# Performance work log

Measured on AMD Instinct MI355X. Metric: run time of the kernel, lower is better.

The kernel has to match this reference:

```python
import jax, jax.numpy as jnp
import numpy as np

H_HT, W_HT = 26, 122      # downsampled pred grid fed to the Hough transform
NUM_ANGLE = 60            # 180 deg / 3 deg
NUM_RHO = 125             # 2*ceil(diag/2)+1, diag = sqrt(26^2+122^2)


def _make_vote_index():
    # Reproduce the structure of vote_index_26_122_3_1.mat: for each pixel
    # (h, w) and angle a, exactly one rho bin receives a vote of 1.0.
    theta = np.deg2rad(np.arange(NUM_ANGLE) * 3.0)
    ys = np.arange(H_HT) - H_HT / 2.0 + 0.5
    xs = np.arange(W_HT) - W_HT / 2.0 + 0.5
    # rho[h, w, a] = x*cos(theta_a) + y*sin(theta_a)
    rho = xs[None, :, None] * np.cos(theta)[None, None, :] \
        + ys[:, None, None] * np.sin(theta)[None, None, :]
    ri = np.clip(np.round(rho).astype(np.int64) + NUM_RHO // 2, 0, NUM_RHO - 1)
    vote = np.zeros((H_HT, W_HT, NUM_ANGLE, NUM_RHO), dtype=np.float32)
    hh, ww, aa = np.meshgrid(np.arange(H_HT), np.arange(W_HT),
                             np.arange(NUM_ANGLE), indexing='ij')
    vote[hh, ww, aa, ri] = 1.0
    return jnp.asarray(vote)


def setup_inputs() -> dict:
    key = jax.random.key(0)
    k1, k2, k3 = jax.random.split(key, 3)
    B, C = 32, 4
    ht = jax.random.uniform(k1, (B, C, NUM_ANGLE, NUM_RHO), dtype=jnp.float32)
    pred = jax.random.uniform(k2, (B, C, 288, 800), dtype=jnp.float32)
    pred_exist = jax.random.uniform(k3, (B, C), dtype=jnp.float32)
    vote_index = _make_vote_index()
    return {"ht": ht, "pred": pred, "pred_exist": pred_exist,
            "vote_index": vote_index}


def _nearest_resize(x, out_h, out_w):
    # torch F.interpolate(mode='nearest'): src = floor(dst * in/out)
    in_h, in_w = x.shape[2], x.shape[3]
    hi = jnp.floor(jnp.arange(out_h) * (in_h / out_h)).astype(jnp.int32)
    wi = jnp.floor(jnp.arange(out_w) * (in_w / out_w)).astype(jnp.int32)
    return x[:, :, hi][:, :, :, wi]


def reference(ht, pred, pred_exist, vote_index):
    B, C = ht.shape[0], ht.shape[1]
    # --- no_grad block in the original ---
    exist = (pred_exist > 0.9).astype(ht.dtype)          # [B, 4]
    exist = jnp.broadcast_to(exist[:, None, :], (B, C, 4))  # [B, C, 4]
    pred_s = _nearest_resize(pred, H_HT, W_HT)           # [B, C, 26, 122]
    # Hough-transform vote accumulation: gather pixel values into (angle, rho)
    # bins via the one-hot vote_index table.
    pred_ht = jnp.einsum('bchw,hwar->bcar', pred_s, vote_index)  # [B,C,A,R]
    idx = jnp.argmax(pred_ht.reshape(B, C, -1), axis=2)  # [B, 4]
    idx = jnp.broadcast_to(idx[:, None, :], (B, C, 4))   # [B, C, 4]
    # --- differentiable part ---
    # F.normalize(ht, dim=2, p=1): L1-normalize along the angle dim.
    l1 = jnp.sum(jnp.abs(ht), axis=2, keepdims=True)
    ht_n = ht / jnp.maximum(l1, 1e-12)
    flat = ht_n.reshape(B, C, -1)                        # [B, C, A*R]
    gathered = jnp.take_along_axis(flat, idx, axis=2)    # [B, C, 4]
    ht_max_log = -jnp.log(gathered + 1e-12)
    loss = ht_max_log * exist
    return loss.mean(axis=2).mean(axis=1)                # [B]
```

## Files before the change

kernel.cpp:

```cpp
#include <hip/hip_runtime.h>
#include <hip/hip_bf16.h>
#include <stdint.h>
#include <math.h>

#define H_HT 26
#define W_HT 122
#define NPIX (H_HT * W_HT)
#define NA 60
#define NR 125
#define NB 32
#define NC 4
#define NBC (NB * NC)
#define PH 288
#define PW 800
#define NSPLIT 16
#define PIX_PT 13

#define TR_BLKS (H_HT * 8)
#define ZERO_BLKS 4

#define WS_OFF   190336
#define WS_LIST  220608
#define WS_PREDT 601280
#define WS_PVP   2225344

__global__ __launch_bounds__(256) void setup(const float* __restrict__ pred,
                                             int* __restrict__ off,
                                             uint16_t* __restrict__ list,
                                             float* __restrict__ pred_T,
                                             unsigned long long* __restrict__ pvp) {
    const int tid = threadIdx.x;
    if (blockIdx.x < NA) {
        const int a = blockIdx.x;
        __shared__ int s_cnt[NR];
        __shared__ int sc[2][NR];
        __shared__ int s_pre[NR + 1];
        __shared__ int s_cur[NR];

        double t  = __dmul_rn((double)(a * 3), 0.017453292519943295);
        double cs = cos(t);
        double sn = sin(t);

        int rloc[PIX_PT];
#pragma unroll
        for (int k = 0; k < PIX_PT; ++k) {
            int p = tid + k * 256;
            rloc[k] = 0;
            if (p < NPIX) {
                int h = p / W_HT;
                int w = p - h * W_HT;
                double xs = (double)w - 60.5;
                double ys = (double)h - 12.5;
                double rho = __dadd_rn(__dmul_rn(xs, cs), __dmul_rn(ys, sn));
                int r = (int)rint(rho) + NR / 2;
                r = r < 0 ? 0 : (r > NR - 1 ? NR - 1 : r);
                rloc[k] = r;
            }
        }
        for (int i = tid; i < NR; i += 256) s_cnt[i] = 0;
        __syncthreads();
#pragma unroll
        for (int k = 0; k < PIX_PT; ++k) {
            int p = tid + k * 256;
            if (p < NPIX) atomicAdd(&s_cnt[rloc[k]], 1);
        }
        __syncthreads();
        if (tid < NR) sc[0][tid] = s_cnt[tid];
        __syncthreads();
        int pin = 0;
        for (int d = 1; d < NR; d <<= 1) {
            if (tid < NR) {
                int v = sc[pin][tid];
                if (tid >= d) v += sc[pin][tid - d];
                sc[pin ^ 1][tid] = v;
            }
            __syncthreads();
            pin ^= 1;
        }
        if (tid == 0) s_pre[0] = 0;
        if (tid < NR) s_pre[tid + 1] = sc[pin][tid];
        __syncthreads();
        for (int r = tid; r < NR + 1; r += 256) off[a * (NR + 1) + r] = s_pre[r];
        for (int r = tid; r < NR; r += 256) s_cur[r] = s_pre[r];
        __syncthreads();
#pragma unroll
        for (int k = 0; k < PIX_PT; ++k) {
            int p = tid + k * 256;
            if (p < NPIX) {
                int slot = atomicAdd(&s_cur[rloc[k]], 1);
                list[a * NPIX + slot] = (uint16_t)p;
            }
        }
    } else if (blockIdx.x < NA + TR_BLKS) {
        const int bidx = blockIdx.x - NA;
        const int h    = bidx >> 3;
        const int g    = bidx & 7;
        const int bc0  = g * 16;
        __shared__ float s_row[16][802];
        const float C1 = (float)(288.0 / 26.0);
        const float C2 = (float)(800.0 / 122.0);
        const int hi = (int)floorf((float)h * C1);
        for (int i = tid; i < 16 * 200; i += 256) {
            int j  = i / 200;
            int c4 = i - j * 200;
            const float4* rp = reinterpret_cast<const float4*>(
                pred + ((size_t)(bc0 + j) * PH + hi) * PW);
            float4 v = rp[c4];
            s_row[j][c4 * 4 + 0] = v.x;
            s_row[j][c4 * 4 + 1] = v.y;
            s_row[j][c4 * 4 + 2] = v.z;
            s_row[j][c4 * 4 + 3] = v.w;
        }
        __syncthreads();
        for (int idx = tid; idx < W_HT * 16; idx += 256) {
            int w = idx >> 4;
            int j = idx & 15;
            int wi = (int)floorf((float)w * C2);
            pred_T[(size_t)(h * W_HT + w) * NBC + bc0 + j] = s_row[j][wi];
        }
    } else {
        int i0 = (blockIdx.x - NA - TR_BLKS) * 256 + tid;
        for (int i = i0; i < NA * NBC; i += ZERO_BLKS * 256) pvp[i] = 0ull;
    }
}

__global__ __launch_bounds__(256) void hough_T4(const float* __restrict__ pred_T,
                                                const int* __restrict__ off,
                                                const uint16_t* __restrict__ list,
                                                unsigned long long* __restrict__ pvp) {
    __shared__ uint16_t s_list[NPIX];
    __shared__ int      s_off[NR + 1];
    __shared__ float    s_v0[4][64], s_v1[4][64];
    __shared__ int      s_i0[4][64], s_i1[4][64];

    const int blk  = blockIdx.x;
    const int a    = blk / NSPLIT;
    const int q    = blk - a * NSPLIT;
    const int tid  = threadIdx.x;
    const int w    = tid >> 6;
    const int lane = tid & 63;

    {
        const uint32_t* src = reinterpret_cast<const uint32_t*>(list + a * NPIX);
        uint32_t* dst = reinterpret_cast<uint32_t*>(s_list);
        for (int i = tid; i < NPIX / 2; i += 256) dst[i] = src[i];
        for (int r = tid; r < NR + 1; r += 256) s_off[r] = off[a * (NR + 1) + r];
    }
    __syncthreads();

    const float2* pT2 = reinterpret_cast<const float2*>(pred_T);
    float bv0 = -1.0f, bv1 = -1.0f; int bi0 = 0x7fffffff, bi1 = 0x7fffffff;
    for (int r = q * 4 + w; r < NR; r += 64) {
        int o0 = s_off[r];
        int o1 = s_off[r + 1];
        float x0 = 0, x1 = 0, x2 = 0, x3 = 0, x4 = 0, x5 = 0, x6 = 0, x7 = 0;
        float y0 = 0, y1 = 0, y2 = 0, y3 = 0, y4 = 0, y5 = 0, y6 = 0, y7 = 0;
        int j = o0;
        for (; j + 8 <= o1; j += 8) {
            float2 v0 = pT2[(int)s_list[j]     * 64 + lane];
            float2 v1 = pT2[(int)s_list[j + 1] * 64 + lane];
            float2 v2 = pT2[(int)s_list[j + 2] * 64 + lane];
            float2 v3 = pT2[(int)s_list[j + 3] * 64 + lane];
            float2 v4 = pT2[(int)s_list[j + 4] * 64 + lane];
            float2 v5 = pT2[(int)s_list[j + 5] * 64 + lane];
            float2 v6 = pT2[(int)s_list[j + 6] * 64 + lane];
            float2 v7 = pT2[(int)s_list[j + 7] * 64 + lane];
            x0 += v0.x; y0 += v0.y; x1 += v1.x; y1 += v1.y;
            x2 += v2.x; y2 += v2.y; x3 += v3.x; y3 += v3.y;
            x4 += v4.x; y4 += v4.y; x5 += v5.x; y5 += v5.y;
            x6 += v6.x; y6 += v6.y; x7 += v7.x; y7 += v7.y;
        }
        for (; j < o1; ++j) {
            float2 v = pT2[(int)s_list[j] * 64 + lane];
            x0 += v.x; y0 += v.y;
        }
        float sx = ((x0 + x1) + (x2 + x3)) + ((x4 + x5) + (x6 + x7));
        float sy = ((y0 + y1) + (y2 + y3)) + ((y4 + y5) + (y6 + y7));
        int gbin = a * NR + r;
        if (sx > bv0) { bv0 = sx; bi0 = gbin; }
        if (sy > bv1) { bv1 = sy; bi1 = gbin; }
    }
    s_v0[w][lane] = bv0; s_i0[w][lane] = bi0;
    s_v1[w][lane] = bv1; s_i1[w][lane] = bi1;
    __syncthreads();
    if (w == 0) {
        float m0 = s_v0[0][lane], m1 = s_v1[0][lane];
        int   j0 = s_i0[0][lane], j1 = s_i1[0][lane];
#pragma unroll
        for (int ww = 1; ww < 4; ++ww) {
            float o0v = s_v0[ww][lane]; int o0i = s_i0[ww][lane];
            float o1v = s_v1[ww][lane]; int o1i = s_i1[ww][lane];
            if (o0v > m0 || (o0v == m0 && o0i < j0)) { m0 = o0v; j0 = o0i; }
            if (o1v > m1 || (o1v == m1 && o1i < j1)) { m1 = o1v; j1 = o1i; }
        }
        unsigned long long e0 = ((unsigned long long)__float_as_uint(m0 < 0.f ? 0.f : m0) << 32)
                              | (unsigned long long)(65535 - j0);
        unsigned long long e1 = ((unsigned long long)__float_as_uint(m1 < 0.f ? 0.f : m1) << 32)
                              | (unsigned long long)(65535 - j1);
        atomicMax(&pvp[(2 * lane)     * NA + a], e0);
        atomicMax(&pvp[(2 * lane + 1) * NA + a], e1);
    }
}

__global__ __launch_bounds__(256) void loss4(const float* __restrict__ ht,
                                             const float* __restrict__ pexist,
                                             const unsigned long long* __restrict__ pvp,
                                             float* __restrict__ out) {
    __shared__ float s_sum[4];
    const int b    = blockIdx.x;
    const int tid  = threadIdx.x;
    const int k    = tid >> 6;
    const int lane = tid & 63;
    const int c    = lane >> 4;
    const int s    = lane & 15;

    unsigned long long be = 0ull;
    if (lane < NA) be = pvp[(b * 4 + k) * NA + lane];
#pragma unroll
    for (int m = 32; m > 0; m >>= 1) {
        unsigned long long oe = __shfl_xor(be, m);
        if (oe > be) be = oe;
    }
    int fidx = 65535 - (int)(be & 0xFFFFull);
    int a0 = fidx / NR;
    int r  = fidx - a0 * NR;

    const float* htc = ht + (size_t)((b * 4 + c) * NA) * NR;
    float acc = 0.0f;
#pragma unroll
    for (int t = 0; t < 4; ++t) {
        int a = s + t * 16;
        if (a < NA) acc += fabsf(htc[a * NR + r]);
    }
#pragma unroll
    for (int m = 1; m < 16; m <<= 1) acc += __shfl_xor(acc, m);

    float term = 0.0f;
    if (s == 0) {
        float l1 = fmaxf(acc, 1e-12f);
        float gg = htc[a0 * NR + r] / l1;
        float ex = (pexist[b * 4 + k] > 0.9f) ? 1.0f : 0.0f;
        term = -logf(gg + 1e-12f) * ex;
    }
#pragma unroll
    for (int m = 16; m < 64; m <<= 1) term += __shfl_xor(term, m);
    if (lane == 0) s_sum[k] = term;
    __syncthreads();
    if (tid == 0)
        out[b] = (s_sum[0] + s_sum[1] + s_sum[2] + s_sum[3]) * (1.0f / 16.0f);
}

extern "C" void kernel_launch(void* const* d_in, const int* in_sizes, int n_in,
                              void* d_out, int out_size, void* d_ws, size_t ws_size,
                              hipStream_t stream) {
    const float* ht     = (const float*)d_in[0];
    const float* pred   = (const float*)d_in[1];
    const float* pexist = (const float*)d_in[2];

    char* ws = (char*)d_ws;
    int*      off    = (int*)     (ws + WS_OFF);
    uint16_t* list   = (uint16_t*)(ws + WS_LIST);
    float*    pred_T = (float*)   (ws + WS_PREDT);
    unsigned long long* pvp = (unsigned long long*)(ws + WS_PVP);

    setup<<<NA + TR_BLKS + ZERO_BLKS, 256, 0, stream>>>(pred, off, list, pred_T, pvp);
    hough_T4<<<NA * NSPLIT, 256, 0, stream>>>(pred_T, off, list, pvp);
    loss4<<<NB, 256, 0, stream>>>(ht, pexist, pvp, (float*)d_out);
}
```

Before: 30.96 us.

## Fuse loss kernel into Hough kernel via last-block atomic counter

Removes the separate loss launch by having the last Hough block to finish, detected with a global atomic counter and thread fences, compute the argmax reduction and loss for all batches. The gather loop is also unrolled from 8 to 16 loads per iteration to keep more memory requests in flight. This trades one kernel launch gap for a serial tail in which a single block does all the loss work, with less parallelism over the ht reads.

Measured after the change: 107.6 us. 248% more time.

```diff
diff --git a/kernel.cpp b/kernel.cpp
--- a/kernel.cpp
+++ b/kernel.cpp
@@ -15,6 +15,7 @@
 #define PW 800
 #define NSPLIT 16
 #define PIX_PT 13
+#define HBLKS (NA * NSPLIT)
 
 #define TR_BLKS (H_HT * 8)
 #define ZERO_BLKS 4
@@ -23,12 +24,14 @@
 #define WS_LIST  220608
 #define WS_PREDT 601280
 #define WS_PVP   2225344
+#define WS_CNT   2286784
 
 __global__ __launch_bounds__(256) void setup(const float* __restrict__ pred,
                                              int* __restrict__ off,
                                              uint16_t* __restrict__ list,
                                              float* __restrict__ pred_T,
-                                             unsigned long long* __restrict__ pvp) {
+                                             unsigned long long* __restrict__ pvp,
+                                             unsigned int* __restrict__ cnt) {
     const int tid = threadIdx.x;
     if (blockIdx.x < NA) {
         const int a = blockIdx.x;
@@ -119,15 +122,21 @@
             pred_T[(size_t)(h * W_HT + w) * NBC + bc0 + j] = s_row[j][wi];
         }
     } else {
-        int i0 = (blockIdx.x - NA - TR_BLKS) * 256 + tid;
+        int bz = blockIdx.x - NA - TR_BLKS;
+        int i0 = bz * 256 + tid;
         for (int i = i0; i < NA * NBC; i += ZERO_BLKS * 256) pvp[i] = 0ull;
+        if (bz == 0 && tid == 0) *cnt = 0u;
     }
 }
 
-__global__ __launch_bounds__(256) void hough_T4(const float* __restrict__ pred_T,
-                                                const int* __restrict__ off,
-                                                const uint16_t* __restrict__ list,
-                                                unsigned long long* __restrict__ pvp) {
+__global__ __launch_bounds__(256) void hough_loss(const float* __restrict__ pred_T,
+                                                  const int* __restrict__ off,
+                                                  const uint16_t* __restrict__ list,
+                                                  unsigned long long* __restrict__ pvp,
+                                                  unsigned int* __restrict__ cnt,
+                                                  const float* __restrict__ ht,
+                                                  const float* __restrict__ pexist,
+                                                  float* __restrict__ out) {
     __shared__ uint16_t s_list[NPIX];
     __shared__ int      s_off[NR + 1];
     __shared__ float    s_v0[4][64], s_v1[4][64];
@@ -153,29 +162,22 @@
     for (int r = q * 4 + w; r < NR; r += 64) {
         int o0 = s_off[r];
         int o1 = s_off[r + 1];
-        float x0 = 0, x1 = 0, x2 = 0, x3 = 0, x4 = 0, x5 = 0, x6 = 0, x7 = 0;
-        float y0 = 0, y1 = 0, y2 = 0, y3 = 0, y4 = 0, y5 = 0, y6 = 0, y7 = 0;
+        float ax[8] = {0,0,0,0,0,0,0,0}, ay[8] = {0,0,0,0,0,0,0,0};
         int j = o0;
-        for (; j + 8 <= o1; j += 8) {
-            float2 v0 = pT2[(int)s_list[j]     * 64 + lane];
-            float2 v1 = pT2[(int)s_list[j + 1] * 64 + lane];
-            float2 v2 = pT2[(int)s_list[j + 2] * 64 + lane];
-            float2 v3 = pT2[(int)s_list[j + 3] * 64 + lane];
-            float2 v4 = pT2[(int)s_list[j + 4] * 64 + lane];
-            float2 v5 = pT2[(int)s_list[j + 5] * 64 + lane];
-            float2 v6 = pT2[(int)s_list[j + 6] * 64 + lane];
-            float2 v7 = pT2[(int)s_list[j + 7] * 64 + lane];
-            x0 += v0.x; y0 += v0.y; x1 += v1.x; y1 += v1.y;
-            x2 += v2.x; y2 += v2.y; x3 += v3.x; y3 += v3.y;
-            x4 += v4.x; y4 += v4.y; x5 += v5.x; y5 += v5.y;
-            x6 += v6.x; y6 += v6.y; x7 += v7.x; y7 += v7.y;
+        for (; j + 16 <= o1; j += 16) {
+            float2 v[16];
+#pragma unroll
+            for (int k = 0; k < 16; ++k)
+                v[k] = pT2[(int)s_list[j + k] * 64 + lane];
+#pragma unroll
+            for (int k = 0; k < 16; ++k) { ax[k & 7] += v[k].x; ay[k & 7] += v[k].y; }
         }
         for (; j < o1; ++j) {
-            float2 v = pT2[(int)s_list[j] * 64 + lane];
-            x0 += v.x; y0 += v.y;
-        }
-        float sx = ((x0 + x1) + (x2 + x3)) + ((x4 + x5) + (x6 + x7));
-        float sy = ((y0 + y1) + (y2 + y3)) + ((y4 + y5) + (y6 + y7));
+            float2 vv = pT2[(int)s_list[j] * 64 + lane];
+            ax[0] += vv.x; ay[0] += vv.y;
+        }
+        float sx = ((ax[0] + ax[1]) + (ax[2] + ax[3])) + ((ax[4] + ax[5]) + (ax[6] + ax[7]));
+        float sy = ((ay[0] + ay[1]) + (ay[2] + ay[3])) + ((ay[4] + ay[5]) + (ay[6] + ay[7]));
         int gbin = a * NR + r;
         if (sx > bv0) { bv0 = sx; bi0 = gbin; }
         if (sy > bv1) { bv1 = sy; bi1 = gbin; }
@@ -200,54 +202,56 @@
         atomicMax(&pvp[(2 * lane)     * NA + a], e0);
         atomicMax(&pvp[(2 * lane + 1) * NA + a], e1);
     }
-}
-
-__global__ __launch_bounds__(256) void loss4(const float* __restrict__ ht,
-                                             const float* __restrict__ pexist,
-                                             const unsigned long long* __restrict__ pvp,
-                                             float* __restrict__ out) {
-    __shared__ float s_sum[4];
-    const int b    = blockIdx.x;
-    const int tid  = threadIdx.x;
-    const int k    = tid >> 6;
-    const int lane = tid & 63;
-    const int c    = lane >> 4;
-    const int s    = lane & 15;
-
-    unsigned long long be = 0ull;
-    if (lane < NA) be = pvp[(b * 4 + k) * NA + lane];
-#pragma unroll
-    for (int m = 32; m > 0; m >>= 1) {
-        unsigned long long oe = __shfl_xor(be, m);
-        if (oe > be) be = oe;
-    }
-    int fidx = 65535 - (int)(be & 0xFFFFull);
-    int a0 = fidx / NR;
-    int r  = fidx - a0 * NR;
-
-    const float* htc = ht + (size_t)((b * 4 + c) * NA) * NR;
-    float acc = 0.0f;
-#pragma unroll
-    for (int t = 0; t < 4; ++t) {
-        int a = s + t * 16;
-        if (a < NA) acc += fabsf(htc[a * NR + r]);
-    }
-#pragma unroll
-    for (int m = 1; m < 16; m <<= 1) acc += __shfl_xor(acc, m);
-
-    float term = 0.0f;
-    if (s == 0) {
+
+    __shared__ unsigned int s_last;
+    __threadfence();
+    __syncthreads();
+    if (tid == 0) s_last = atomicAdd(cnt, 1u);
+    __syncthreads();
+    if (s_last != (unsigned int)(HBLKS - 1)) return;
+    __threadfence();
+
+    __shared__ int   s_fidx[NBC];
+    __shared__ float s_t1[256], s_t2[256];
+
+    if (tid < NBC) {
+        unsigned long long be = 0ull;
+        const unsigned long long* pr = pvp + tid * NA;
+        for (int aa = 0; aa < NA; ++aa) {
+            unsigned long long e = pr[aa];
+            if (e > be) be = e;
+        }
+        s_fidx[tid] = 65535 - (int)(be & 0xFFFFull);
+    }
+    __syncthreads();
+
+#pragma unroll
+    for (int it = 0; it < 2; ++it) {
+        int T = tid + 256 * it;
+        int b = T >> 4;
+        int combo = T & 15;
+        int c = combo >> 2;
+        int k = combo & 3;
+        int fidx = s_fidx[b * 4 + k];
+        int a0 = fidx / NR;
+        int r  = fidx - a0 * NR;
+        const float* htc = ht + (size_t)((b * 4 + c) * NA) * NR;
+        float acc = 0.0f;
+        for (int aa = 0; aa < NA; ++aa) acc += fabsf(htc[aa * NR + r]);
         float l1 = fmaxf(acc, 1e-12f);
         float gg = htc[a0 * NR + r] / l1;
         float ex = (pexist[b * 4 + k] > 0.9f) ? 1.0f : 0.0f;
-        term = -logf(gg + 1e-12f) * ex;
-    }
-#pragma unroll
-    for (int m = 16; m < 64; m <<= 1) term += __shfl_xor(term, m);
-    if (lane == 0) s_sum[k] = term;
-    __syncthreads();
-    if (tid == 0)
-        out[b] = (s_sum[0] + s_sum[1] + s_sum[2] + s_sum[3]) * (1.0f / 16.0f);
+        float term = -logf(gg + 1e-12f) * ex;
+        if (it == 0) s_t1[tid] = term; else s_t2[tid] = term;
+    }
+    __syncthreads();
+    if (tid < 32) {
+        int b = tid;
+        float s = 0.0f;
+        if (b < 16) { for (int i = 0; i < 16; ++i) s += s_t1[b * 16 + i]; }
+        else        { for (int i = 0; i < 16; ++i) s += s_t2[(b - 16) * 16 + i]; }
+        out[b] = s * (1.0f / 16.0f);
+    }
 }
 
 extern "C" void kernel_launch(void* const* d_in, const int* in_sizes, int n_in,
@@ -262,8 +266,8 @@
     uint16_t* list   = (uint16_t*)(ws + WS_LIST);
     float*    pred_T = (float*)   (ws + WS_PREDT);
     unsigned long long* pvp = (unsigned long long*)(ws + WS_PVP);
-
-    setup<<<NA + TR_BLKS + ZERO_BLKS, 256, 0, stream>>>(pred, off, list, pred_T, pvp);
-    hough_T4<<<NA * NSPLIT, 256, 0, stream>>>(pred_T, off, list, pvp);
-    loss4<<<NB, 256, 0, stream>>>(ht, pexist, pvp, (float*)d_out);
+    unsigned int* cnt = (unsigned int*)(ws + WS_CNT);
+
+    setup<<<NA + TR_BLKS + ZERO_BLKS, 256, 0, stream>>>(pred, off, list, pred_T, pvp, cnt);
+    hough_loss<<<HBLKS, 256, 0, stream>>>(pred_T, off, list, pvp, cnt, ht, pexist, (float*)d_out);
 }
```

## Gather float4 per lane and split rho bin pixel lists across half-waves

Applied to the files above, without the earlier changes.

The Hough vote kernel now has each lane load a float4 (four batch-channel columns) instead of a float2, so 32 lanes cover the 128 columns. The two half-waves each take a different 8-pixel chunk of the bin's list, and their partial sums are combined with a cross-half shuffle. The tail loop is replaced by masked FMA with clamped indices. The goal is wider loads and more gathers in flight per wave, at the cost of masked wasted loads on short bins plus extra shuffle and reduction work.

Measured after the change: 30.08 us, median of 2. -2.8%, faster.

```diff
diff --git a/kernel.cpp b/kernel.cpp
--- a/kernel.cpp
+++ b/kernel.cpp
@@ -119,19 +119,20 @@
             pred_T[(size_t)(h * W_HT + w) * NBC + bc0 + j] = s_row[j][wi];
         }
     } else {
-        int i0 = (blockIdx.x - NA - TR_BLKS) * 256 + tid;
+        int bz = blockIdx.x - NA - TR_BLKS;
+        int i0 = bz * 256 + tid;
         for (int i = i0; i < NA * NBC; i += ZERO_BLKS * 256) pvp[i] = 0ull;
     }
 }
 
-__global__ __launch_bounds__(256) void hough_T4(const float* __restrict__ pred_T,
+__global__ __launch_bounds__(256) void hough_T7(const float* __restrict__ pred_T,
                                                 const int* __restrict__ off,
                                                 const uint16_t* __restrict__ list,
                                                 unsigned long long* __restrict__ pvp) {
     __shared__ uint16_t s_list[NPIX];
     __shared__ int      s_off[NR + 1];
-    __shared__ float    s_v0[4][64], s_v1[4][64];
-    __shared__ int      s_i0[4][64], s_i1[4][64];
+    __shared__ float    s_v[4][32][4];
+    __shared__ int      s_i[4][32][4];
 
     const int blk  = blockIdx.x;
     const int a    = blk / NSPLIT;
@@ -139,6 +140,8 @@
     const int tid  = threadIdx.x;
     const int w    = tid >> 6;
     const int lane = tid & 63;
+    const int li   = lane & 31;
+    const int hw8  = (lane >> 5) * 8;
 
     {
         const uint32_t* src = reinterpret_cast<const uint32_t*>(list + a * NPIX);
@@ -148,57 +151,95 @@
     }
     __syncthreads();
 
-    const float2* pT2 = reinterpret_cast<const float2*>(pred_T);
-    float bv0 = -1.0f, bv1 = -1.0f; int bi0 = 0x7fffffff, bi1 = 0x7fffffff;
+    const float4* pT4 = reinterpret_cast<const float4*>(pred_T);
+    float bvx = -1.0f, bvy = -1.0f, bvz = -1.0f, bvw = -1.0f;
+    int   bix = 0, biy = 0, biz = 0, biw = 0;
     for (int r = q * 4 + w; r < NR; r += 64) {
-        int o0 = s_off[r];
-        int o1 = s_off[r + 1];
-        float x0 = 0, x1 = 0, x2 = 0, x3 = 0, x4 = 0, x5 = 0, x6 = 0, x7 = 0;
-        float y0 = 0, y1 = 0, y2 = 0, y3 = 0, y4 = 0, y5 = 0, y6 = 0, y7 = 0;
-        int j = o0;
-        for (; j + 8 <= o1; j += 8) {
-            float2 v0 = pT2[(int)s_list[j]     * 64 + lane];
-            float2 v1 = pT2[(int)s_list[j + 1] * 64 + lane];
-            float2 v2 = pT2[(int)s_list[j + 2] * 64 + lane];
-            float2 v3 = pT2[(int)s_list[j + 3] * 64 + lane];
-            float2 v4 = pT2[(int)s_list[j + 4] * 64 + lane];
-            float2 v5 = pT2[(int)s_list[j + 5] * 64 + lane];
-            float2 v6 = pT2[(int)s_list[j + 6] * 64 + lane];
-            float2 v7 = pT2[(int)s_list[j + 7] * 64 + lane];
-            x0 += v0.x; y0 += v0.y; x1 += v1.x; y1 += v1.y;
-            x2 += v2.x; y2 += v2.y; x3 += v3.x; y3 += v3.y;
-            x4 += v4.x; y4 += v4.y; x5 += v5.x; y5 += v5.y;
-            x6 += v6.x; y6 += v6.y; x7 += v7.x; y7 += v7.y;
-        }
-        for (; j < o1; ++j) {
-            float2 v = pT2[(int)s_list[j] * 64 + lane];
-            x0 += v.x; y0 += v.y;
-        }
-        float sx = ((x0 + x1) + (x2 + x3)) + ((x4 + x5) + (x6 + x7));
-        float sy = ((y0 + y1) + (y2 + y3)) + ((y4 + y5) + (y6 + y7));
+        const int o0 = s_off[r];
+        const int o1 = s_off[r + 1];
+        float4 c0 = {0,0,0,0}, c1 = {0,0,0,0}, c2 = {0,0,0,0}, c3 = {0,0,0,0};
+        float4 c4 = {0,0,0,0}, c5 = {0,0,0,0}, c6 = {0,0,0,0}, c7 = {0,0,0,0};
+        for (int j = o0; j < o1; j += 16) {
+            int base = j + hw8;
+            int i0 = base, i1 = base + 1, i2 = base + 2, i3 = base + 3;
+            int i4 = base + 4, i5 = base + 5, i6 = base + 6, i7 = base + 7;
+            float m0 = (i0 < o1) ? 1.0f : 0.0f;
+            float m1 = (i1 < o1) ? 1.0f : 0.0f;
+            float m2 = (i2 < o1) ? 1.0f : 0.0f;
+            float m3 = (i3 < o1) ? 1.0f : 0.0f;
+            float m4 = (i4 < o1) ? 1.0f : 0.0f;
+            float m5 = (i5 < o1) ? 1.0f : 0.0f;
+            float m6 = (i6 < o1) ? 1.0f : 0.0f;
+            float m7 = (i7 < o1) ? 1.0f : 0.0f;
+            int p0 = s_list[i0 < o1 ? i0 : o0];
+            int p1 = s_list[i1 < o1 ? i1 : o0];
+            int p2 = s_list[i2 < o1 ? i2 : o0];
+            int p3 = s_list[i3 < o1 ? i3 : o0];
+            int p4 = s_list[i4 < o1 ? i4 : o0];
+            int p5 = s_list[i5 < o1 ? i5 : o0];
+            int p6 = s_list[i6 < o1 ? i6 : o0];
+            int p7 = s_list[i7 < o1 ? i7 : o0];
+            float4 v0 = pT4[p0 * 32 + li];
+            float4 v1 = pT4[p1 * 32 + li];
+            float4 v2 = pT4[p2 * 32 + li];
+            float4 v3 = pT4[p3 * 32 + li];
+            float4 v4 = pT4[p4 * 32 + li];
+            float4 v5 = pT4[p5 * 32 + li];
+            float4 v6 = pT4[p6 * 32 + li];
+            float4 v7 = pT4[p7 * 32 + li];
+            c0.x = fmaf(v0.x, m0, c0.x); c0.y = fmaf(v0.y, m0, c0.y);
+            c0.z = fmaf(v0.z, m0, c0.z); c0.w = fmaf(v0.w, m0, c0.w);
+            c1.x = fmaf(v1.x, m1, c1.x); c1.y = fmaf(v1.y, m1, c1.y);
+            c1.z = fmaf(v1.z, m1, c1.z); c1.w = fmaf(v1.w, m1, c1.w);
+            c2.x = fmaf(v2.x, m2, c2.x); c2.y = fmaf(v2.y, m2, c2.y);
+            c2.z = fmaf(v2.z, m2, c2.z); c2.w = fmaf(v2.w, m2, c2.w);
+            c3.x = fmaf(v3.x, m3, c3.x); c3.y = fmaf(v3.y, m3, c3.y);
+            c3.z = fmaf(v3.z, m3, c3.z); c3.w = fmaf(v3.w, m3, c3.w);
+            c4.x = fmaf(v4.x, m4, c4.x); c4.y = fmaf(v4.y, m4, c4.y);
+            c4.z = fmaf(v4.z, m4, c4.z); c4.w = fmaf(v4.w, m4, c4.w);
+            c5.x = fmaf(v5.x, m5, c5.x); c5.y = fmaf(v5.y, m5, c5.y);
+            c5.z = fmaf(v5.z, m5, c5.z); c5.w = fmaf(v5.w, m5, c5.w);
+            c6.x = fmaf(v6.x, m6, c6.x); c6.y = fmaf(v6.y, m6, c6.y);
+            c6.z = fmaf(v6.z, m6, c6.z); c6.w = fmaf(v6.w, m6, c6.w);
+            c7.x = fmaf(v7.x, m7, c7.x); c7.y = fmaf(v7.y, m7, c7.y);
+            c7.z = fmaf(v7.z, m7, c7.z); c7.w = fmaf(v7.w, m7, c7.w);
+        }
+        float sx = ((c0.x + c1.x) + (c2.x + c3.x)) + ((c4.x + c5.x) + (c6.x + c7.x));
+        float sy = ((c0.y + c1.y) + (c2.y + c3.y)) + ((c4.y + c5.y) + (c6.y + c7.y));
+        float sz = ((c0.z + c1.z) + (c2.z + c3.z)) + ((c4.z + c5.z) + (c6.z + c7.z));
+        float sw = ((c0.w + c1.w) + (c2.w + c3.w)) + ((c4.w + c5.w) + (c6.w + c7.w));
+        sx += __shfl_xor(sx, 32);
+        sy += __shfl_xor(sy, 32);
+        sz += __shfl_xor(sz, 32);
+        sw += __shfl_xor(sw, 32);
         int gbin = a * NR + r;
-        if (sx > bv0) { bv0 = sx; bi0 = gbin; }
-        if (sy > bv1) { bv1 = sy; bi1 = gbin; }
-    }
-    s_v0[w][lane] = bv0; s_i0[w][lane] = bi0;
-    s_v1[w][lane] = bv1; s_i1[w][lane] = bi1;
+        if (sx > bvx) { bvx = sx; bix = gbin; }
+        if (sy > bvy) { bvy = sy; biy = gbin; }
+        if (sz > bvz) { bvz = sz; biz = gbin; }
+        if (sw > bvw) { bvw = sw; biw = gbin; }
+    }
+    if (hw8 == 0) {
+        s_v[w][li][0] = bvx; s_i[w][li][0] = bix;
+        s_v[w][li][1] = bvy; s_i[w][li][1] = biy;
+        s_v[w][li][2] = bvz; s_i[w][li][2] = biz;
+        s_v[w][li][3] = bvw; s_i[w][li][3] = biw;
+    }
     __syncthreads();
-    if (w == 0) {
-        float m0 = s_v0[0][lane], m1 = s_v1[0][lane];
-        int   j0 = s_i0[0][lane], j1 = s_i1[0][lane];
-#pragma unroll
-        for (int ww = 1; ww < 4; ++ww) {
-            float o0v = s_v0[ww][lane]; int o0i = s_i0[ww][lane];
-            float o1v = s_v1[ww][lane]; int o1i = s_i1[ww][lane];
-            if (o0v > m0 || (o0v == m0 && o0i < j0)) { m0 = o0v; j0 = o0i; }
-            if (o1v > m1 || (o1v == m1 && o1i < j1)) { m1 = o1v; j1 = o1i; }
-        }
-        unsigned long long e0 = ((unsigned long long)__float_as_uint(m0 < 0.f ? 0.f : m0) << 32)
-                              | (unsigned long long)(65535 - j0);
-        unsigned long long e1 = ((unsigned long long)__float_as_uint(m1 < 0.f ? 0.f : m1) << 32)
-                              | (unsigned long long)(65535 - j1);
-        atomicMax(&pvp[(2 * lane)     * NA + a], e0);
-        atomicMax(&pvp[(2 * lane + 1) * NA + a], e1);
+    if (tid < 32) {
+#pragma unroll
+        for (int comp = 0; comp < 4; ++comp) {
+            float m = s_v[0][tid][comp];
+            int   jb = s_i[0][tid][comp];
+#pragma unroll
+            for (int ww = 1; ww < 4; ++ww) {
+                float ov = s_v[ww][tid][comp];
+                int   oi = s_i[ww][tid][comp];
+                if (ov > m || (ov == m && oi < jb)) { m = ov; jb = oi; }
+            }
+            unsigned long long e = ((unsigned long long)__float_as_uint(m < 0.f ? 0.f : m) << 32)
+                                 | (unsigned long long)(65535 - jb);
+            atomicMax(&pvp[(4 * tid + comp) * NA + a], e);
+        }
     }
 }
 
@@ -264,6 +305,6 @@
     unsigned long long* pvp = (unsigned long long*)(ws + WS_PVP);
 
     setup<<<NA + TR_BLKS + ZERO_BLKS, 256, 0, stream>>>(pred, off, list, pred_T, pvp);
-    hough_T4<<<NA * NSPLIT, 256, 0, stream>>>(pred_T, off, list, pvp);
+    hough_T7<<<NA * NSPLIT, 256, 0, stream>>>(pred_T, off, list, pvp);
     loss4<<<NB, 256, 0, stream>>>(ht, pexist, pvp, (float*)d_out);
 }
```
